# Performance work log

Measured on AMD Instinct MI355X. Metric: run time of the kernel, lower is better.

The kernel has to match this reference:

```python
import jax, jax.numpy as jnp
import numpy as np

N_NODES = 100000
N_EDGES = 3200000
D_IN = 64
D_OUT = 64


def setup_inputs() -> dict:
    key = jax.random.key(0)
    k0, k1, k2, k3 = jax.random.split(key, 4)
    x = jax.random.normal(k0, (N_NODES, D_IN), dtype=jnp.float32)
    edge_index = jax.random.randint(k1, (2, N_EDGES), 0, N_NODES, dtype=jnp.int64)
    edge_weight = jax.random.uniform(k2, (N_EDGES,), dtype=jnp.float32)
    W = jax.random.normal(k3, (D_IN, D_OUT), dtype=jnp.float32) / jnp.sqrt(jnp.float32(D_IN))
    b = jnp.zeros((D_OUT,), dtype=jnp.float32)
    return {"x": x, "edge_index": edge_index, "edge_weight": edge_weight, "W": W, "b": b}


def reference(x, edge_index, edge_weight, W, b):
    # GiGCNConv forward: asymmetric (random-walk, D^-1 A) gcn_norm with self loops,
    # then GCNConv(normalize=False): linear -> edge-weighted scatter-add -> bias.
    N = x.shape[0]
    src, dst = edge_index[0], edge_index[1]

    # add self loops (fill value 1.0 since improved=False)
    loop = jnp.arange(N, dtype=src.dtype)
    src = jnp.concatenate([src, loop])
    dst = jnp.concatenate([dst, loop])
    ew = jnp.concatenate([edge_weight.astype(x.dtype), jnp.ones((N,), dtype=x.dtype)])

    # asymmetric normalization: in-degree (at dst) inverse scaling
    deg = jax.ops.segment_sum(ew, dst, num_segments=N)          # [N]
    deg_inv = jnp.where(deg > 0, 1.0 / deg, 0.0)                # inf -> 0
    norm = deg_inv[dst] * ew                                    # [E+N]

    # GCNConv: project then aggregate messages at destination nodes
    h = x @ W                                                   # [N, D_OUT]
    msg = norm[:, None] * h[src]                                # [E+N, D_OUT] gather
    out = jax.ops.segment_sum(msg, dst, num_segments=N)         # scatter-add
    return out + b
```

## Files before the change

### kernel.cpp

```cpp
#include <hip/hip_runtime.h>


#define D 64
#define BSH 9
#define NPB 512
#define MAXB1 256
#define BATCHA 4096
#define C1S 32
#define WSCALE 8192.0f
#define WINV (1.0f / 8192.0f)

static __device__ __forceinline__ unsigned short f2bf(float f) {
    unsigned u = __float_as_uint(f);
    u += 0x7FFFu + ((u >> 16) & 1u);
    return (unsigned short)(u >> 16);
}
static __device__ __forceinline__ float bflo(unsigned u) {
    return __uint_as_float(u << 16);
}
static __device__ __forceinline__ float bfhi(unsigned u) {
    return __uint_as_float(u & 0xFFFF0000u);
}


__global__ __launch_bounds__(256) void hist_kernel(const int* __restrict__ dst,
                                                   int* __restrict__ hist, int E, int B1) {
    __shared__ int lh[MAXB1];
    int tid = threadIdx.x;
    if (tid < MAXB1) lh[tid] = 0;
    __syncthreads();
    int t = blockIdx.x * 256 + tid;
    int stride = gridDim.x * 256;
    if ((E & 3) == 0 && (((size_t)dst & 15) == 0)) {
        const int4* d4 = (const int4*)dst;
        int n4 = E >> 2;
        for (int e = t; e < n4; e += stride) {
            int4 v = d4[e];
            atomicAdd(&lh[v.x >> BSH], 1);
            atomicAdd(&lh[v.y >> BSH], 1);
            atomicAdd(&lh[v.z >> BSH], 1);
            atomicAdd(&lh[v.w >> BSH], 1);
        }
    } else {
        for (int e = t; e < E; e += stride) {
            int d = __builtin_nontemporal_load(dst + e);
            atomicAdd(&lh[d >> BSH], 1);
        }
    }
    __syncthreads();
    if (tid < B1) {
        int v = lh[tid];
        if (v) atomicAdd(&hist[tid], v);
    }
}


__global__ __launch_bounds__(256) void scan_kernel(const int* __restrict__ hist,
                                                   int* __restrict__ off1,
                                                   int* __restrict__ cur1, int B1, int E) {
    __shared__ int s[256];
    int tid = threadIdx.x;
    int v = (tid < B1) ? hist[tid] : 0;
    s[tid] = v;
    __syncthreads();
    for (int o = 1; o < 256; o <<= 1) {
        int t = (tid >= o) ? s[tid - o] : 0;
        __syncthreads();
        s[tid] += t;
        __syncthreads();
    }
    if (tid < B1) {
        int ex = s[tid] - v;
        off1[tid] = ex;
        cur1[tid * C1S] = ex;
    }
    if (tid == 0) off1[B1] = E;
}


__global__ __launch_bounds__(512) void partgemm_kernel(const int* __restrict__ src,
                                                       const int* __restrict__ dst,
                                                       const float* __restrict__ ew,
                                                       int* __restrict__ cur1,
                                                       int2* __restrict__ pairs1,
                                                       int E, int nb, int aligned, int gA,
                                                       const float* __restrict__ x,
                                                       const float* __restrict__ W,
                                                       unsigned short* __restrict__ hbf,
                                                       int N) {
    __shared__ union SM {
        struct { int bcnt[MAXB1]; int bbase[MAXB1]; int brank[MAXB1]; } p;
        struct { float Ws[D * D]; float xs[64][D]; } g;
    } sm;
    int tid = threadIdx.x;

    if ((int)blockIdx.x < gA) {
        for (int ib = blockIdx.x; ib < nb; ib += gA) {
            int base = ib * BATCHA;
            int blen = E - base;
            if (blen > BATCHA) blen = BATCHA;
            if (tid < MAXB1) { sm.p.bcnt[tid] = 0; sm.p.brank[tid] = 0; }
            __syncthreads();
            int dv[8], sv[8];
            float wv[8];
            int off = tid * 8;
            if (aligned && off + 8 <= blen) {
#pragma unroll
                for (int kk = 0; kk < 2; ++kk) {
                    int4 d4 = ((const int4*)(dst + base + off))[kk];
                    int4 s4 = ((const int4*)(src + base + off))[kk];
                    float4 w4 = ((const float4*)(ew + base + off))[kk];
                    dv[kk * 4 + 0] = d4.x; dv[kk * 4 + 1] = d4.y;
                    dv[kk * 4 + 2] = d4.z; dv[kk * 4 + 3] = d4.w;
                    sv[kk * 4 + 0] = s4.x; sv[kk * 4 + 1] = s4.y;
                    sv[kk * 4 + 2] = s4.z; sv[kk * 4 + 3] = s4.w;
                    wv[kk * 4 + 0] = w4.x; wv[kk * 4 + 1] = w4.y;
                    wv[kk * 4 + 2] = w4.z; wv[kk * 4 + 3] = w4.w;
                }
#pragma unroll
                for (int m = 0; m < 8; ++m) atomicAdd(&sm.p.bcnt[dv[m] >> BSH], 1);
            } else {
#pragma unroll
                for (int m = 0; m < 8; ++m) {
                    bool v = (off + m) < blen;
                    int e = base + off + m;
                    dv[m] = v ? __builtin_nontemporal_load(dst + e) : -1;
                    sv[m] = v ? __builtin_nontemporal_load(src + e) : 0;
                    wv[m] = v ? __builtin_nontemporal_load(ew + e) : 0.0f;
                    if (v) atomicAdd(&sm.p.bcnt[dv[m] >> BSH], 1);
                }
            }
            __syncthreads();
            if (tid < MAXB1 && sm.p.bcnt[tid] > 0)
                sm.p.bbase[tid] = atomicAdd(&cur1[tid * C1S], sm.p.bcnt[tid]);
            __syncthreads();
#pragma unroll
            for (int m = 0; m < 8; ++m) {
                if (dv[m] >= 0) {
                    int bin = dv[m] >> BSH;
                    int r = atomicAdd(&sm.p.brank[bin], 1);
                    pairs1[sm.p.bbase[bin] + r] =
                        make_int2(sv[m] | ((dv[m] & (NPB - 1)) << 17),
                                  __float_as_int(wv[m]));
                }
            }
            __syncthreads();
        }
    } else {
        int j = tid & 63;
        int g = tid >> 6;
        int base = ((int)blockIdx.x - gA) * 64;
        for (int i = tid; i < D * D; i += 512) sm.g.Ws[i] = W[i];
        for (int rr = g; rr < 64; rr += 8) {
            int r = base + rr;
            if (r < N) sm.g.xs[rr][j] = x[(size_t)r * D + j];
        }
        __syncthreads();
        float wc[D];
#pragma unroll
        for (int k = 0; k < D; ++k) wc[k] = sm.g.Ws[k * D + j];
        for (int rr = g; rr < 64; rr += 8) {
            int r = base + rr;
            if (r < N) {
                float s0 = 0.0f, s1 = 0.0f, s2 = 0.0f, s3 = 0.0f;
#pragma unroll
                for (int k = 0; k < D; k += 4) {
                    s0 = fmaf(sm.g.xs[rr][k + 0], wc[k + 0], s0);
                    s1 = fmaf(sm.g.xs[rr][k + 1], wc[k + 1], s1);
                    s2 = fmaf(sm.g.xs[rr][k + 2], wc[k + 2], s2);
                    s3 = fmaf(sm.g.xs[rr][k + 3], wc[k + 3], s3);
                }
                hbf[(size_t)r * D + j] = f2bf((s0 + s1) + (s2 + s3));
            }
        }
    }
}


__global__ __launch_bounds__(512) void sortmerge_kernel(const int2* __restrict__ pairs1,
                                                        const int* __restrict__ off1,
                                                        unsigned* __restrict__ cw,
                                                        int* __restrict__ node_off,
                                                        int N, int B1) {
    __shared__ int lh[NPB];
    __shared__ int s[NPB];
    __shared__ int cur[NPB];
    int tid = threadIdx.x;
    int c = blockIdx.x;
    int e0 = off1[c], e1 = off1[c + 1];

    lh[tid] = 0;
    __syncthreads();

    for (int ib = e0; ib < e1; ib += 512 * 8) {
        long long pv[8];
#pragma unroll
        for (int m = 0; m < 8; ++m) {
            int i = ib + m * 512 + tid;
            pv[m] = (i < e1)
                ? __builtin_nontemporal_load((const long long*)(pairs1 + i))
                : -1LL;
        }
#pragma unroll
        for (int m = 0; m < 8; ++m) {
            int i = ib + m * 512 + tid;
            if (i < e1) atomicAdd(&lh[((int)pv[m] >> 17) & (NPB - 1)], 1);
        }
    }
    __syncthreads();

    s[tid] = lh[tid];
    __syncthreads();
    for (int o = 1; o < NPB; o <<= 1) {
        int t = (tid >= o) ? s[tid - o] : 0;
        __syncthreads();
        s[tid] += t;
        __syncthreads();
    }
    int ex = s[tid] - lh[tid];
    int gbase = c << BSH;
    if (gbase + tid <= N) node_off[gbase + tid] = e0 + ex;
    if (c == B1 - 1 && tid == 0) node_off[N] = e1;
    cur[tid] = ex;
    __syncthreads();

    for (int ib = e0; ib < e1; ib += 512 * 8) {
        long long pv[8];
#pragma unroll
        for (int m = 0; m < 8; ++m) {
            int i = ib + m * 512 + tid;
            pv[m] = (i < e1)
                ? __builtin_nontemporal_load((const long long*)(pairs1 + i))
                : -1LL;
        }
#pragma unroll
        for (int m = 0; m < 8; ++m) {
            int i = ib + m * 512 + tid;
            if (i < e1) {
                int px = (int)pv[m];
                float w = __int_as_float((int)(pv[m] >> 32));
                int node = (px >> 17) & (NPB - 1);
                int pos = atomicAdd(&cur[node], 1);
                int wq = (int)fminf(fmaxf(w, 0.0f) * WSCALE + 0.5f, 32767.0f);
                cw[e0 + pos] = (unsigned)(px & 0x1FFFF) | ((unsigned)wq << 17);
            }
        }
    }
}


__global__ __launch_bounds__(256) void accum_kernel(const unsigned* __restrict__ cw,
                                                    const int* __restrict__ node_off,
                                                    const unsigned short* __restrict__ hbf,
                                                    const float* __restrict__ bias,
                                                    float* __restrict__ out, int N) {
    int t = blockIdx.x * 256 + threadIdx.x;
    int n = t >> 6;
    int l = t & 63;
    if (n >= N) return;
    int eg = l >> 4;
    int cl = l & 15;
    int base = node_off[n];
    int cnt = node_off[n + 1] - base;
    const unsigned* pp = cw + base;
    const unsigned short* hcol = hbf + cl * 4;

    float a0 = 0.0f, a1 = 0.0f, a2 = 0.0f, a3 = 0.0f;
    float degs = 0.0f;
    int i = eg;
    for (; i + 12 < cnt; i += 16) {
        unsigned va = pp[i];
        unsigned vb = pp[i + 4];
        unsigned vc = pp[i + 8];
        unsigned vd = pp[i + 12];
        uint2 ha = *(const uint2*)(hcol + (size_t)(va & 0x1FFFF) * D);
        uint2 hb = *(const uint2*)(hcol + (size_t)(vb & 0x1FFFF) * D);
        uint2 hc = *(const uint2*)(hcol + (size_t)(vc & 0x1FFFF) * D);
        uint2 hd = *(const uint2*)(hcol + (size_t)(vd & 0x1FFFF) * D);
        float wa = (float)(va >> 17) * WINV;
        float wb = (float)(vb >> 17) * WINV;
        float wc = (float)(vc >> 17) * WINV;
        float wd = (float)(vd >> 17) * WINV;
        degs += (wa + wb) + (wc + wd);
        a0 = fmaf(wa, bflo(ha.x), a0);
        a1 = fmaf(wa, bfhi(ha.x), a1);
        a2 = fmaf(wa, bflo(ha.y), a2);
        a3 = fmaf(wa, bfhi(ha.y), a3);
        a0 = fmaf(wb, bflo(hb.x), a0);
        a1 = fmaf(wb, bfhi(hb.x), a1);
        a2 = fmaf(wb, bflo(hb.y), a2);
        a3 = fmaf(wb, bfhi(hb.y), a3);
        a0 = fmaf(wc, bflo(hc.x), a0);
        a1 = fmaf(wc, bfhi(hc.x), a1);
        a2 = fmaf(wc, bflo(hc.y), a2);
        a3 = fmaf(wc, bfhi(hc.y), a3);
        a0 = fmaf(wd, bflo(hd.x), a0);
        a1 = fmaf(wd, bfhi(hd.x), a1);
        a2 = fmaf(wd, bflo(hd.y), a2);
        a3 = fmaf(wd, bfhi(hd.y), a3);
    }
    for (; i < cnt; i += 4) {
        unsigned v = pp[i];
        uint2 hv = *(const uint2*)(hcol + (size_t)(v & 0x1FFFF) * D);
        float w = (float)(v >> 17) * WINV;
        degs += w;
        a0 = fmaf(w, bflo(hv.x), a0);
        a1 = fmaf(w, bfhi(hv.x), a1);
        a2 = fmaf(w, bflo(hv.y), a2);
        a3 = fmaf(w, bfhi(hv.y), a3);
    }

    a0 += __shfl_xor(a0, 16); a0 += __shfl_xor(a0, 32);
    a1 += __shfl_xor(a1, 16); a1 += __shfl_xor(a1, 32);
    a2 += __shfl_xor(a2, 16); a2 += __shfl_xor(a2, 32);
    a3 += __shfl_xor(a3, 16); a3 += __shfl_xor(a3, 32);
    degs += __shfl_xor(degs, 16); degs += __shfl_xor(degs, 32);

    if (eg == 0) {
        uint2 hs = *(const uint2*)(hcol + (size_t)n * D);
        a0 += bflo(hs.x);
        a1 += bfhi(hs.x);
        a2 += bflo(hs.y);
        a3 += bfhi(hs.y);
        degs += 1.0f;
        float di = 1.0f / degs;
        const float4 bv = *(const float4*)(bias + cl * 4);
        float4 o;
        o.x = fmaf(di, a0, bv.x);
        o.y = fmaf(di, a1, bv.y);
        o.z = fmaf(di, a2, bv.z);
        o.w = fmaf(di, a3, bv.w);
        __builtin_nontemporal_store(o.x, out + (size_t)n * D + cl * 4 + 0);
        __builtin_nontemporal_store(o.y, out + (size_t)n * D + cl * 4 + 1);
        __builtin_nontemporal_store(o.z, out + (size_t)n * D + cl * 4 + 2);
        __builtin_nontemporal_store(o.w, out + (size_t)n * D + cl * 4 + 3);
    }
}


__global__ __launch_bounds__(256) void deg_kernel(const int* __restrict__ dst,
                                                  const float* __restrict__ ew,
                                                  float* __restrict__ deg, int E) {
    int t = blockIdx.x * 256 + threadIdx.x;
    int stride = gridDim.x * 256;
    for (int e = t; e < E; e += stride) atomicAdd(&deg[dst[e]], ew[e]);
}

__global__ __launch_bounds__(256) void deginv_kernel(float* __restrict__ deg, int N) {
    int t = blockIdx.x * 256 + threadIdx.x;
    int stride = gridDim.x * 256;
    for (int n = t; n < N; n += stride) {
        float tot = deg[n] + 1.0f;
        deg[n] = (tot > 0.0f) ? (1.0f / tot) : 0.0f;
    }
}

__global__ __launch_bounds__(256) void gemm16f_kernel(const float* __restrict__ x,
                                                      const float* __restrict__ W,
                                                      float* __restrict__ h, int N) {
    __shared__ float Ws[D * D];
    __shared__ float xs[16][D];
    int tid = threadIdx.x;
    int j = tid & 63;
    int q = tid >> 6;
    int base = blockIdx.x * 16;
    for (int i = tid; i < D * D; i += 256) Ws[i] = W[i];
    for (int rr = q; rr < 16; rr += 4) {
        int r = base + rr;
        if (r < N) xs[rr][j] = x[(size_t)r * D + j];
    }
    __syncthreads();
    for (int rr = q; rr < 16; rr += 4) {
        int r = base + rr;
        if (r < N) {
            float sum = 0.0f;
#pragma unroll
            for (int k = 0; k < D; ++k) sum = fmaf(xs[rr][k], Ws[k * D + j], sum);
            h[(size_t)r * D + j] = sum;
        }
    }
}

__global__ __launch_bounds__(256) void init_kernel(const float* __restrict__ h,
                                                   const float* __restrict__ deginv,
                                                   const float* __restrict__ b,
                                                   float* __restrict__ out, int N) {
    int t = blockIdx.x * 256 + threadIdx.x;
    int stride = gridDim.x * 256;
    int nq = N * (D / 4);
    const float4* h4 = (const float4*)h;
    const float4* b4 = (const float4*)b;
    float4* o4 = (float4*)out;
    for (int q = t; q < nq; q += stride) {
        int n = q >> 4;
        int c4 = q & 15;
        float4 hv = h4[q];
        float4 bv = b4[c4];
        float di = deginv[n];
        float4 o;
        o.x = bv.x + di * hv.x;
        o.y = bv.y + di * hv.y;
        o.z = bv.z + di * hv.z;
        o.w = bv.w + di * hv.w;
        o4[q] = o;
    }
}

__global__ __launch_bounds__(256) void scatter_kernel(const int* __restrict__ src,
                                                      const int* __restrict__ dst,
                                                      const float* __restrict__ ew,
                                                      const float* __restrict__ deginv,
                                                      const float* __restrict__ h,
                                                      float* __restrict__ out, int E) {
    int t = blockIdx.x * 256 + threadIdx.x;
    int wave = t >> 6;
    int lane = t & 63;
    int nwaves = (gridDim.x * 256) >> 6;
    for (int e = wave; e < E; e += nwaves) {
        int s = src[e];
        int d = dst[e];
        float norm = deginv[d] * ew[e];
        atomicAdd(&out[d * D + lane], norm * h[s * D + lane]);
    }
}


extern "C" void kernel_launch(void* const* d_in, const int* in_sizes, int n_in,
                              void* d_out, int out_size, void* d_ws, size_t ws_size,
                              hipStream_t stream) {
    const float* x  = (const float*)d_in[0];
    const int*   ei = (const int*)d_in[1];
    const float* ew = (const float*)d_in[2];
    const float* W  = (const float*)d_in[3];
    const float* b  = (const float*)d_in[4];
    float* out = (float*)d_out;

    int N = in_sizes[0] / D;
    int E = in_sizes[2];
    const int* srcp = ei;
    const int* dstp = ei + E;

    int B1 = (N + NPB - 1) >> BSH;

    size_t ints_n = 256 + 320 + (size_t)MAXB1 * C1S + ((size_t)N + 64);
    size_t p1_off  = ((ints_n * 4) + 255) & ~(size_t)255;
    size_t hbf_off = (p1_off + (size_t)E * 8 + 255) & ~(size_t)255;
    size_t cw_off  = (hbf_off + (size_t)N * D * 2 + 255) & ~(size_t)255;
    size_t need = cw_off + (size_t)E * 4;

    if (N <= 131072 && ws_size >= need) {
        int* hist     = (int*)d_ws;
        int* off1     = hist + 256;
        int* cur1     = off1 + 320;
        int* node_off = cur1 + (size_t)MAXB1 * C1S;
        int2* pairs1  = (int2*)((char*)d_ws + p1_off);
        unsigned short* hbf = (unsigned short*)((char*)d_ws + hbf_off);
        unsigned* cw  = (unsigned*)((char*)d_ws + cw_off);

        int aligned = (((E & 3) == 0) && (((size_t)dstp & 15) == 0)) ? 1 : 0;

        hipMemsetAsync(hist, 0, 256 * 4, stream);
        hist_kernel<<<512, 256, 0, stream>>>(dstp, hist, E, B1);
        scan_kernel<<<1, 256, 0, stream>>>(hist, off1, cur1, B1, E);
        int nb = (E + BATCHA - 1) / BATCHA;
        int gA = nb < 2048 ? nb : 2048;
        int gG = (N + 63) / 64;
        partgemm_kernel<<<gA + gG, 512, 0, stream>>>(srcp, dstp, ew, cur1, pairs1,
                                                     E, nb, aligned, gA, x, W, hbf, N);
        sortmerge_kernel<<<B1, 512, 0, stream>>>(pairs1, off1, cw, node_off, N, B1);
        accum_kernel<<<(N + 3) / 4, 256, 0, stream>>>(cw, node_off, hbf, b, out, N);
    } else {
        size_t Npad = ((size_t)N + 63) & ~(size_t)63;
        float* deg = (float*)d_ws;
        float* h = deg + Npad;
        hipMemsetAsync(deg, 0, (size_t)N * sizeof(float), stream);
        deg_kernel<<<2048, 256, 0, stream>>>(dstp, ew, deg, E);
        deginv_kernel<<<(N + 255) / 256, 256, 0, stream>>>(deg, N);
        gemm16f_kernel<<<(N + 15) / 16, 256, 0, stream>>>(x, W, h, N);
        init_kernel<<<2048, 256, 0, stream>>>(h, deg, b, out, N);
        scatter_kernel<<<2048, 256, 0, stream>>>(srcp, dstp, ew, deg, h, out, E);
    }
}
```

Before: 181.9 us.

## Stage binned edge pairs in shared memory for coalesced global scatter

The partition pass now records each edge's rank from the first LDS atomic, computes a block-local prefix scan of bin counts, and places pairs into a shared-memory tile sorted by bin. A second loop then writes the tile to global memory in index order, so consecutive threads write consecutive addresses within each bin run. This replaces the second round of LDS atomics and the scattered global stores. In exchange it adds a 256-entry scan with many barriers and about 36KB of extra shared memory, which may lower occupancy.

```diff
diff --git a/kernel.cpp b/kernel.cpp
--- a/kernel.cpp
+++ b/kernel.cpp
@@ -89,7 +89,14 @@
                                                        unsigned short* __restrict__ hbf,
                                                        int N) {
     __shared__ union SM {
-        struct { int bcnt[MAXB1]; int bbase[MAXB1]; int brank[MAXB1]; } p;
+        struct {
+            int2 tile[BATCHA];
+            unsigned char binof[BATCHA];
+            int bcnt[MAXB1];
+            int lbase[MAXB1];
+            int bbase[MAXB1];
+            int scan_[MAXB1];
+        } p;
         struct { float Ws[D * D]; float xs[64][D]; } g;
     } sm;
     int tid = threadIdx.x;
@@ -99,9 +106,10 @@
             int base = ib * BATCHA;
             int blen = E - base;
             if (blen > BATCHA) blen = BATCHA;
-            if (tid < MAXB1) { sm.p.bcnt[tid] = 0; sm.p.brank[tid] = 0; }
+            if (tid < MAXB1) sm.p.bcnt[tid] = 0;
             __syncthreads();
-            int dv[8], sv[8];
+
+            int bv[8], sv[8], rv[8];
             float wv[8];
             int off = tid * 8;
             if (aligned && off + 8 <= blen) {
@@ -110,39 +118,70 @@
                     int4 d4 = ((const int4*)(dst + base + off))[kk];
                     int4 s4 = ((const int4*)(src + base + off))[kk];
                     float4 w4 = ((const float4*)(ew + base + off))[kk];
-                    dv[kk * 4 + 0] = d4.x; dv[kk * 4 + 1] = d4.y;
-                    dv[kk * 4 + 2] = d4.z; dv[kk * 4 + 3] = d4.w;
-                    sv[kk * 4 + 0] = s4.x; sv[kk * 4 + 1] = s4.y;
-                    sv[kk * 4 + 2] = s4.z; sv[kk * 4 + 3] = s4.w;
-                    wv[kk * 4 + 0] = w4.x; wv[kk * 4 + 1] = w4.y;
-                    wv[kk * 4 + 2] = w4.z; wv[kk * 4 + 3] = w4.w;
+                    int dd[4] = {d4.x, d4.y, d4.z, d4.w};
+                    int ss[4] = {s4.x, s4.y, s4.z, s4.w};
+                    float ww[4] = {w4.x, w4.y, w4.z, w4.w};
+#pragma unroll
+                    for (int q = 0; q < 4; ++q) {
+                        int m = kk * 4 + q;
+                        sv[m] = ss[q] | ((dd[q] & (NPB - 1)) << 17);
+                        wv[m] = ww[q];
+                        bv[m] = dd[q] >> BSH;
+                    }
                 }
 #pragma unroll
-                for (int m = 0; m < 8; ++m) atomicAdd(&sm.p.bcnt[dv[m] >> BSH], 1);
+                for (int m = 0; m < 8; ++m)
+                    rv[m] = atomicAdd(&sm.p.bcnt[bv[m]], 1);
             } else {
 #pragma unroll
                 for (int m = 0; m < 8; ++m) {
                     bool v = (off + m) < blen;
                     int e = base + off + m;
-                    dv[m] = v ? __builtin_nontemporal_load(dst + e) : -1;
-                    sv[m] = v ? __builtin_nontemporal_load(src + e) : 0;
-                    wv[m] = v ? __builtin_nontemporal_load(ew + e) : 0.0f;
-                    if (v) atomicAdd(&sm.p.bcnt[dv[m] >> BSH], 1);
+                    if (v) {
+                        int d = __builtin_nontemporal_load(dst + e);
+                        int s = __builtin_nontemporal_load(src + e);
+                        float w = __builtin_nontemporal_load(ew + e);
+                        sv[m] = s | ((d & (NPB - 1)) << 17);
+                        wv[m] = w;
+                        bv[m] = d >> BSH;
+                        rv[m] = atomicAdd(&sm.p.bcnt[bv[m]], 1);
+                    } else {
+                        bv[m] = -1;
+                    }
                 }
             }
             __syncthreads();
-            if (tid < MAXB1 && sm.p.bcnt[tid] > 0)
-                sm.p.bbase[tid] = atomicAdd(&cur1[tid * C1S], sm.p.bcnt[tid]);
+
+            if (tid < MAXB1) sm.p.scan_[tid] = sm.p.bcnt[tid];
             __syncthreads();
+            for (int o = 1; o < MAXB1; o <<= 1) {
+                int t = 0;
+                if (tid < MAXB1 && tid >= o) t = sm.p.scan_[tid - o];
+                __syncthreads();
+                if (tid < MAXB1) sm.p.scan_[tid] += t;
+                __syncthreads();
+            }
+            if (tid < MAXB1) {
+                sm.p.lbase[tid] = sm.p.scan_[tid] - sm.p.bcnt[tid];
+                if (sm.p.bcnt[tid] > 0)
+                    sm.p.bbase[tid] = atomicAdd(&cur1[tid * C1S], sm.p.bcnt[tid]);
+            }
+            __syncthreads();
+
 #pragma unroll
             for (int m = 0; m < 8; ++m) {
-                if (dv[m] >= 0) {
-                    int bin = dv[m] >> BSH;
-                    int r = atomicAdd(&sm.p.brank[bin], 1);
-                    pairs1[sm.p.bbase[bin] + r] =
-                        make_int2(sv[m] | ((dv[m] & (NPB - 1)) << 17),
-                                  __float_as_int(wv[m]));
+                if (bv[m] >= 0) {
+                    int slot = sm.p.lbase[bv[m]] + rv[m];
+                    sm.p.tile[slot] = make_int2(sv[m], __float_as_int(wv[m]));
+                    sm.p.binof[slot] = (unsigned char)bv[m];
                 }
+            }
+            __syncthreads();
+
+            for (int i = tid; i < blen; i += 512) {
+                int2 p = sm.p.tile[i];
+                int bin = sm.p.binof[i];
+                pairs1[sm.p.bbase[bin] + (i - sm.p.lbase[bin])] = p;
             }
             __syncthreads();
         }
```

Result: faster. 176.0 us (-3.3%).
